# Kernel tuning notes

Measured on AMD Instinct MI355X. Metric: run time of the kernel, lower is better.

The kernel has to match this reference:

```python
import jax, jax.numpy as jnp
import numpy as np

B, N, C = 2, 384, 128
D = C // 4          # bottleneck_dim
H = 128             # time_mlp_hidden_dim


def setup_inputs() -> dict:
    key = jax.random.key(0)
    ks = jax.random.split(key, 12)
    s = 0.02
    return {
        "edge_embed": jax.random.normal(ks[0], (B, N, N, C), jnp.float32),
        "edge_mask": jax.random.randint(ks[1], (B, N, N), 0, 2, jnp.int32),
        "r3_t": jax.random.uniform(ks[2], (B,), jnp.float32),
        # linear params stored as [in, out]
        "Wg": jax.random.normal(ks[3], (C, D), jnp.float32) * s,
        "bg": jnp.zeros((D,), jnp.float32),
        "Wv": jax.random.normal(ks[4], (C, D), jnp.float32) * s,
        "bv": jnp.zeros((D,), jnp.float32),
        "Wd": jax.random.normal(ks[5], (C, D), jnp.float32) * s,
        "bd": jnp.zeros((D,), jnp.float32),
        "Wo": jax.random.normal(ks[6], (D, C), jnp.float32) * s,
        "bo": jnp.zeros((C,), jnp.float32),
        "W1": jax.random.normal(ks[7], (1, H), jnp.float32) * s,
        "b1": jnp.zeros((H,), jnp.float32),
        "W2": jax.random.normal(ks[8], (H, 2 * C), jnp.float32) * s,
        "b2": jnp.zeros((2 * C,), jnp.float32),
    }


def reference(edge_embed, edge_mask, r3_t, Wg, bg, Wv, bv, Wd, bd, Wo, bo, W1, b1, W2, b2):
    Bb, Nn, _, Cc = edge_embed.shape
    P = edge_embed.reshape(Bb, Nn * Nn, Cc)          # [B, N^2, C]
    m = (edge_mask.reshape(Bb, Nn * Nn, 1) != 0)
    mf = m.astype(P.dtype)

    fP = P @ Wg + bg                                 # [B, N^2, D]
    gP = P @ Wv + bv                                 # [B, N^2, D]
    fP = jnp.where(m, fP, jnp.asarray(-1e8, P.dtype))
    w = jax.nn.softmax(fP, axis=1)                   # softmax over all edges
    w = w * mf
    w = w / (w.sum(axis=1, keepdims=True) + 1e-8)

    V = jnp.einsum('bnd,bne->bde', w, gP)            # [B, D, D] global context

    hP = jax.nn.softmax(P @ Wd + bd, axis=2)         # softmax over channels
    O = jnp.einsum('bnd,bde->bne', hP, V)            # redistribute
    O = (O @ Wo + bo).reshape(Bb, Nn, Nn, Cc)

    # FiLM conditioned on timestep (torch GELU is exact erf form)
    t = r3_t.reshape(Bb, 1)
    t_emb = jax.nn.gelu(t @ W1 + b1, approximate=False) @ W2 + b2
    scale, shift = jnp.split(t_emb, 2, axis=-1)
    O = O * (1 + scale[:, None, None, :]) + shift[:, None, None, :]

    return edge_embed + O
```

## Files before the change

### kernel.cpp

```cpp
#include <hip/hip_runtime.h>
#include <hip/hip_bf16.h>
#include <math.h>

#define N2 147456
#define CC 128
#define TILES 2304

#define WS_VACC  0
#define WS_S     2048
#define WS_FS    2112
#define WS_SH    2368
#define WS_UPACK 2624
#define WS_B2P   6720

typedef __attribute__((ext_vector_type(8))) __bf16 bf16x8;
typedef __attribute__((ext_vector_type(4))) __bf16 bf16x4;
typedef __attribute__((ext_vector_type(4))) float f32x4;

#define MFMA16(a_, b_, c_) __builtin_amdgcn_mfma_f32_16x16x32_bf16((a_), (b_), (c_), 0, 0, 0)

__global__ __launch_bounds__(256) void k0_init(
    const float* __restrict__ r3t,
    const float* __restrict__ W1, const float* __restrict__ b1,
    const float* __restrict__ W2, const float* __restrict__ b2,
    float* __restrict__ ws)
{
    const int t = threadIdx.x, bx = blockIdx.x;
    if (bx > 0) {
        const int i = (bx - 1) * 256 + t;
        if (i < 2112) ws[i] = 0.0f;
        return;
    }
    __shared__ float h[2][128];
    {
        const int b = t >> 7, j = t & 127;
        const float x = r3t[b] * W1[j] + b1[j];
        h[b][j] = 0.5f * x * (1.0f + erff(x * 0.7071067811865475f));
    }
    __syncthreads();
    const int j2 = t;
    float acc0 = b2[j2], acc1 = b2[j2];
    for (int k = 0; k < 128; ++k) {
        const float w2 = W2[k * 256 + j2];
        acc0 += h[0][k] * w2;
        acc1 += h[1][k] * w2;
    }
    if (j2 < 128) {
        ws[WS_FS + j2]       = 1.0f + acc0;
        ws[WS_FS + 128 + j2] = 1.0f + acc1;
    } else {
        ws[WS_SH + (j2 - 128)]       = acc0;
        ws[WS_SH + 128 + (j2 - 128)] = acc1;
    }
}

__global__ __launch_bounds__(256, 3) void k1_accum(
    const float* __restrict__ P, const int* __restrict__ mask,
    const float* __restrict__ Wg, const float* __restrict__ bg,
    const float* __restrict__ Wv, const float* __restrict__ bv,
    float* __restrict__ ws)
{
    __shared__ __bf16 ef_t[32][72];
    __shared__ __bf16 gv_t[32][72];

    const int t  = threadIdx.x;
    const int b  = blockIdx.y;
    const int w  = t >> 6;
    const int l  = t & 63;
    const int lr = l & 15;
    const int lg = l >> 4;

    bf16x8 wfrag[2][2][4];
    #pragma unroll
    for (int nt = 0; nt < 2; ++nt)
      #pragma unroll
      for (int ks = 0; ks < 4; ++ks) {
        const int base = (ks * 32 + 8 * lg) * 32 + nt * 16 + lr;
        bf16x8 f0, f1;
        #pragma unroll
        for (int i = 0; i < 8; ++i) {
            f0[i] = (__bf16)Wg[base + i * 32];
            f1[i] = (__bf16)Wv[base + i * 32];
        }
        wfrag[0][nt][ks] = f0;
        wfrag[1][nt][ks] = f1;
      }
    const float bgv[2] = { bg[lr], bg[lr + 16] };
    const float bvv[2] = { bv[lr], bv[lr + 16] };

    const int mt = w >> 1, ntq = w & 1;
    f32x4 vacc = {0.f, 0.f, 0.f, 0.f};
    float accS = 0.f;
    const int sd = t >> 3, ss = t & 7;

    const float* Pb = P + (size_t)b * N2 * CC;
    const int*   mb = mask + (size_t)b * N2;

    for (int tile = blockIdx.x; tile < TILES; tile += gridDim.x) {
        const int row0 = tile * 64 + w * 16;
        const float* prow = Pb + (size_t)(row0 + lr) * CC + 8 * lg;

        bf16x8 afrag[4];
        #pragma unroll
        for (int ks = 0; ks < 4; ++ks) {
            const float4 a0 = *(const float4*)(prow + ks * 32);
            const float4 a1 = *(const float4*)(prow + ks * 32 + 4);
            bf16x8 f;
            f[0] = (__bf16)a0.x; f[1] = (__bf16)a0.y; f[2] = (__bf16)a0.z; f[3] = (__bf16)a0.w;
            f[4] = (__bf16)a1.x; f[5] = (__bf16)a1.y; f[6] = (__bf16)a1.z; f[7] = (__bf16)a1.w;
            afrag[ks] = f;
        }

        f32x4 facc0 = {0,0,0,0}, facc1 = {0,0,0,0}, gacc0 = {0,0,0,0}, gacc1 = {0,0,0,0};
        #pragma unroll
        for (int ks = 0; ks < 4; ++ks) {
            facc0 = MFMA16(afrag[ks], wfrag[0][0][ks], facc0);
            facc1 = MFMA16(afrag[ks], wfrag[0][1][ks], facc1);
            gacc0 = MFMA16(afrag[ks], wfrag[1][0][ks], gacc0);
            gacc1 = MFMA16(afrag[ks], wfrag[1][1][ks], gacc1);
        }

        const int4 mk4 = *(const int4*)&mb[row0 + lg * 4];
        const int mk[4] = { mk4.x, mk4.y, mk4.z, mk4.w };

        bf16x4 pe0, pe1, pg0, pg1;
        #pragma unroll
        for (int r = 0; r < 4; ++r) {
            pe0[r] = (__bf16)(mk[r] ? __expf(facc0[r] + bgv[0]) : 0.0f);
            pe1[r] = (__bf16)(mk[r] ? __expf(facc1[r] + bgv[1]) : 0.0f);
            pg0[r] = (__bf16)(gacc0[r] + bvv[0]);
            pg1[r] = (__bf16)(gacc1[r] + bvv[1]);
        }
        const int cbase = w * 16 + lg * 4;
        *(bf16x4*)&ef_t[lr     ][cbase] = pe0;
        *(bf16x4*)&ef_t[lr + 16][cbase] = pe1;
        *(bf16x4*)&gv_t[lr     ][cbase] = pg0;
        *(bf16x4*)&gv_t[lr + 16][cbase] = pg1;
        __syncthreads();

        #pragma unroll
        for (int ks = 0; ks < 2; ++ks) {
            const bf16x8 ea = *(const bf16x8*)&ef_t[mt  * 16 + lr][ks * 32 + 8 * lg];
            const bf16x8 gb = *(const bf16x8*)&gv_t[ntq * 16 + lr][ks * 32 + 8 * lg];
            vacc = MFMA16(ea, gb, vacc);
        }
        {
            const bf16x8 ev = *(const bf16x8*)&ef_t[sd][ss * 8];
            float s = 0.f;
            #pragma unroll
            for (int i = 0; i < 8; ++i) s += (float)ev[i];
            accS += s;
        }
        __syncthreads();
    }

    #pragma unroll
    for (int r = 0; r < 4; ++r) {
        const int d = mt * 16 + lg * 4 + r;
        const int e = ntq * 16 + lr;
        atomicAdd(ws + WS_VACC + b * 1024 + d * 32 + e, vacc[r]);
    }
    accS += __shfl_xor(accS, 1);
    accS += __shfl_xor(accS, 2);
    accS += __shfl_xor(accS, 4);
    if (ss == 0) atomicAdd(ws + WS_S + b * 32 + sd, accS);
}

__global__ __launch_bounds__(256) void k2_mid(
    const float* __restrict__ Wo, const float* __restrict__ bo,
    float* __restrict__ ws)
{
    __shared__ float V[1024];
    __shared__ float wo[32][128];
    __shared__ float fs[128];
    const int t = threadIdx.x, b = blockIdx.x;

    if (t < 128) fs[t] = ws[WS_FS + b * 128 + t];
    #pragma unroll
    for (int i = 0; i < 4; ++i) {
        const int idx = t + i * 256;
        const int d = idx >> 5;
        const float s = ws[WS_S + b * 32 + d];
        V[idx] = ws[WS_VACC + b * 1024 + idx] / (s * (1.0f + 1e-8f));
    }
    #pragma unroll
    for (int i = 0; i < 4; ++i) {
        const int j = t + i * 256;
        ((float4*)&wo[0][0])[j] = ((const float4*)Wo)[j];
    }
    __syncthreads();

    const int c = t & 127, dh = t >> 7;
    float wcol[32];
    #pragma unroll
    for (int e = 0; e < 32; ++e) wcol[e] = wo[e][c];
    const float fsc = fs[c];
    if (dh == 0) ws[WS_B2P + b * 128 + c] = bo[c] * fsc + ws[WS_SH + b * 128 + c];

    __bf16* dst = (__bf16*)(ws + WS_UPACK);
    #pragma unroll
    for (int dd = 0; dd < 16; ++dd) {
        const int d = dh * 16 + dd;
        float acc = 0.0f;
        #pragma unroll
        for (int e = 0; e < 32; ++e) acc += V[d * 32 + e] * wcol[e];
        acc *= fsc;
        const int lg = d >> 3, ii = d & 7, nt = c >> 4, lr = c & 15;
        dst[(((size_t)b * 8 + nt) * 64 + (lg * 16 + lr)) * 8 + ii] = (__bf16)acc;
    }
}

__global__ __launch_bounds__(256, 3) void k3_out(
    const float* __restrict__ P,
    const float* __restrict__ Wd, const float* __restrict__ bd,
    const float* __restrict__ ws, float* __restrict__ out)
{
    __shared__ __bf16 h_t[64][40];

    const int t  = threadIdx.x;
    const int b  = blockIdx.y;
    const int w  = t >> 6, l = t & 63, lr = l & 15, lg = l >> 4;

    bf16x8 ufrag[8];
    {
        const bf16x8* up = (const bf16x8*)(ws + WS_UPACK) + (size_t)b * 512 + l;
        #pragma unroll
        for (int nt = 0; nt < 8; ++nt) ufrag[nt] = up[nt * 64];
    }
    float b2v[8][4];
    #pragma unroll
    for (int nt = 0; nt < 8; ++nt) {
        const float4 v = *(const float4*)(ws + WS_B2P + b * 128 + nt * 16 + lg * 4);
        b2v[nt][0] = v.x; b2v[nt][1] = v.y; b2v[nt][2] = v.z; b2v[nt][3] = v.w;
    }
    bf16x8 wdfrag[2][4];
    #pragma unroll
    for (int nt = 0; nt < 2; ++nt)
      #pragma unroll
      for (int ks = 0; ks < 4; ++ks) {
        const int base = (ks * 32 + 8 * lg) * 32 + nt * 16 + lr;
        bf16x8 f;
        #pragma unroll
        for (int i = 0; i < 8; ++i) f[i] = (__bf16)Wd[base + i * 32];
        wdfrag[nt][ks] = f;
      }
    float bdv[8];
    #pragma unroll
    for (int r = 0; r < 4; ++r) {
        bdv[r]     = bd[lg * 4 + r];
        bdv[4 + r] = bd[16 + lg * 4 + r];
    }

    const float* Pb = P + (size_t)b * N2 * CC;
    float*       Ob = out + (size_t)b * N2 * CC;

    for (int tile = TILES - 1 - blockIdx.x; tile >= 0; tile -= gridDim.x) {
        const int row0 = tile * 64 + w * 16;
        const size_t rbase = (size_t)(row0 + lr) * CC;
        const float* prow = Pb + rbase + 8 * lg;

        bf16x8 afrag[4];
        #pragma unroll
        for (int ks = 0; ks < 4; ++ks) {
            const float4 a0 = *(const float4*)(prow + ks * 32);
            const float4 a1 = *(const float4*)(prow + ks * 32 + 4);
            bf16x8 f;
            f[0] = (__bf16)a0.x; f[1] = (__bf16)a0.y; f[2] = (__bf16)a0.z; f[3] = (__bf16)a0.w;
            f[4] = (__bf16)a1.x; f[5] = (__bf16)a1.y; f[6] = (__bf16)a1.z; f[7] = (__bf16)a1.w;
            afrag[ks] = f;
        }

        f32x4 dacc0 = {0,0,0,0}, dacc1 = {0,0,0,0};
        #pragma unroll
        for (int ks = 0; ks < 4; ++ks) {
            dacc0 = MFMA16(wdfrag[0][ks], afrag[ks], dacc0);
            dacc1 = MFMA16(wdfrag[1][ks], afrag[ks], dacc1);
        }

        float v[8];
        #pragma unroll
        for (int r = 0; r < 4; ++r) {
            v[r]     = dacc0[r] + bdv[r];
            v[4 + r] = dacc1[r] + bdv[4 + r];
        }
        float m = v[0];
        #pragma unroll
        for (int j = 1; j < 8; ++j) m = fmaxf(m, v[j]);
        m = fmaxf(m, __shfl_xor(m, 16));
        m = fmaxf(m, __shfl_xor(m, 32));
        float e[8], s = 0.f;
        #pragma unroll
        for (int j = 0; j < 8; ++j) { e[j] = __expf(v[j] - m); s += e[j]; }
        s += __shfl_xor(s, 16);
        s += __shfl_xor(s, 32);
        const float inv = 1.0f / s;

        bf16x4 h0, h1;
        #pragma unroll
        for (int r = 0; r < 4; ++r) {
            h0[r] = (__bf16)(e[r] * inv);
            h1[r] = (__bf16)(e[4 + r] * inv);
        }
        const int hrow = w * 16 + lr;
        *(bf16x4*)&h_t[hrow][lg * 4]      = h0;
        *(bf16x4*)&h_t[hrow][16 + lg * 4] = h1;
        const bf16x8 hf = *(const bf16x8*)&h_t[hrow][8 * lg];

        #pragma unroll
        for (int nt = 0; nt < 8; ++nt) {
            f32x4 ci;
            ci[0] = b2v[nt][0]; ci[1] = b2v[nt][1]; ci[2] = b2v[nt][2]; ci[3] = b2v[nt][3];
            const f32x4 oacc = MFMA16(ufrag[nt], hf, ci);
            const size_t off = rbase + nt * 16 + lg * 4;
            const float4 p4 = *(const float4*)(Pb + off);
            float4 o4;
            o4.x = p4.x + oacc[0]; o4.y = p4.y + oacc[1];
            o4.z = p4.z + oacc[2]; o4.w = p4.w + oacc[3];
            *(float4*)(Ob + off) = o4;
        }
    }
}

extern "C" void kernel_launch(void* const* d_in, const int* in_sizes, int n_in,
                              void* d_out, int out_size, void* d_ws, size_t ws_size,
                              hipStream_t stream) {
    const float* P   = (const float*)d_in[0];
    const int*   msk = (const int*)d_in[1];
    const float* r3t = (const float*)d_in[2];
    const float* Wg  = (const float*)d_in[3];
    const float* bg  = (const float*)d_in[4];
    const float* Wv  = (const float*)d_in[5];
    const float* bv  = (const float*)d_in[6];
    const float* Wd  = (const float*)d_in[7];
    const float* bd  = (const float*)d_in[8];
    const float* Wo  = (const float*)d_in[9];
    const float* bo  = (const float*)d_in[10];
    const float* W1  = (const float*)d_in[11];
    const float* b1  = (const float*)d_in[12];
    const float* W2  = (const float*)d_in[13];
    const float* b2  = (const float*)d_in[14];
    float* ws  = (float*)d_ws;
    float* out = (float*)d_out;

    hipLaunchKernelGGL(k0_init,  dim3(10),      dim3(256), 0, stream, r3t, W1, b1, W2, b2, ws);
    hipLaunchKernelGGL(k1_accum, dim3(384, 2),  dim3(256), 0, stream, P, msk, Wg, bg, Wv, bv, ws);
    hipLaunchKernelGGL(k2_mid,   dim3(2),       dim3(256), 0, stream, Wo, bo, ws);
    hipLaunchKernelGGL(k3_out,   dim3(768, 2),  dim3(256), 0, stream, P, Wd, bd, ws, out);
}
```

Before: 117.6 us.

## Fold time-MLP into mid kernel, memset workspace, prefetch next P tile in output kernel

Removes the separate init kernel: the workspace is zeroed with hipMemsetAsync and the FiLM time-MLP (GELU plus W2 projection) is now computed inside k2_mid into shared memory. In k3_out, the P rows for the next tile are loaded into registers while the current tile is converted and processed, so global load latency overlaps with MFMA and softmax work. The prefetch raises register pressure under the 3-blocks-per-CU launch bound. The memset may still count as a launch of its own.

```diff
diff --git a/kernel.cpp b/kernel.cpp
--- a/kernel.cpp
+++ b/kernel.cpp
@@ -8,8 +8,6 @@
 
 #define WS_VACC  0
 #define WS_S     2048
-#define WS_FS    2112
-#define WS_SH    2368
 #define WS_UPACK 2624
 #define WS_B2P   6720
 
@@ -18,41 +16,6 @@
 typedef __attribute__((ext_vector_type(4))) float f32x4;
 
 #define MFMA16(a_, b_, c_) __builtin_amdgcn_mfma_f32_16x16x32_bf16((a_), (b_), (c_), 0, 0, 0)
-
-__global__ __launch_bounds__(256) void k0_init(
-    const float* __restrict__ r3t,
-    const float* __restrict__ W1, const float* __restrict__ b1,
-    const float* __restrict__ W2, const float* __restrict__ b2,
-    float* __restrict__ ws)
-{
-    const int t = threadIdx.x, bx = blockIdx.x;
-    if (bx > 0) {
-        const int i = (bx - 1) * 256 + t;
-        if (i < 2112) ws[i] = 0.0f;
-        return;
-    }
-    __shared__ float h[2][128];
-    {
-        const int b = t >> 7, j = t & 127;
-        const float x = r3t[b] * W1[j] + b1[j];
-        h[b][j] = 0.5f * x * (1.0f + erff(x * 0.7071067811865475f));
-    }
-    __syncthreads();
-    const int j2 = t;
-    float acc0 = b2[j2], acc1 = b2[j2];
-    for (int k = 0; k < 128; ++k) {
-        const float w2 = W2[k * 256 + j2];
-        acc0 += h[0][k] * w2;
-        acc1 += h[1][k] * w2;
-    }
-    if (j2 < 128) {
-        ws[WS_FS + j2]       = 1.0f + acc0;
-        ws[WS_FS + 128 + j2] = 1.0f + acc1;
-    } else {
-        ws[WS_SH + (j2 - 128)]       = acc0;
-        ws[WS_SH + 128 + (j2 - 128)] = acc1;
-    }
-}
 
 __global__ __launch_bounds__(256, 3) void k1_accum(
     const float* __restrict__ P, const int* __restrict__ mask,
@@ -167,15 +130,23 @@
 }
 
 __global__ __launch_bounds__(256) void k2_mid(
+    const float* __restrict__ r3t,
+    const float* __restrict__ W1, const float* __restrict__ b1,
+    const float* __restrict__ W2, const float* __restrict__ b2,
     const float* __restrict__ Wo, const float* __restrict__ bo,
     float* __restrict__ ws)
 {
     __shared__ float V[1024];
     __shared__ float wo[32][128];
+    __shared__ float h[128];
     __shared__ float fs[128];
+    __shared__ float sh[128];
     const int t = threadIdx.x, b = blockIdx.x;
 
-    if (t < 128) fs[t] = ws[WS_FS + b * 128 + t];
+    if (t < 128) {
+        const float x = r3t[b] * W1[t] + b1[t];
+        h[t] = 0.5f * x * (1.0f + erff(x * 0.7071067811865475f));
+    }
     #pragma unroll
     for (int i = 0; i < 4; ++i) {
         const int idx = t + i * 256;
@@ -190,12 +161,20 @@
     }
     __syncthreads();
 
+    {
+        float acc = b2[t];
+        for (int k = 0; k < 128; ++k) acc += h[k] * W2[k * 256 + t];
+        if (t < 128) fs[t] = 1.0f + acc;
+        else         sh[t - 128] = acc;
+    }
+    __syncthreads();
+
     const int c = t & 127, dh = t >> 7;
     float wcol[32];
     #pragma unroll
     for (int e = 0; e < 32; ++e) wcol[e] = wo[e][c];
     const float fsc = fs[c];
-    if (dh == 0) ws[WS_B2P + b * 128 + c] = bo[c] * fsc + ws[WS_SH + b * 128 + c];
+    if (dh == 0) ws[WS_B2P + b * 128 + c] = bo[c] * fsc + sh[c];
 
     __bf16* dst = (__bf16*)(ws + WS_UPACK);
     #pragma unroll
@@ -253,21 +232,40 @@
 
     const float* Pb = P + (size_t)b * N2 * CC;
     float*       Ob = out + (size_t)b * N2 * CC;
-
-    for (int tile = TILES - 1 - blockIdx.x; tile >= 0; tile -= gridDim.x) {
+    const int step = gridDim.x;
+
+    int tile = TILES - 1 - blockIdx.x;
+    float4 a4[8];
+    {
+        const float* prow = Pb + (size_t)(tile * 64 + w * 16 + lr) * CC + 8 * lg;
+        #pragma unroll
+        for (int ks = 0; ks < 4; ++ks) {
+            a4[2 * ks]     = *(const float4*)(prow + ks * 32);
+            a4[2 * ks + 1] = *(const float4*)(prow + ks * 32 + 4);
+        }
+    }
+
+    for (; tile >= 0; tile -= step) {
         const int row0 = tile * 64 + w * 16;
         const size_t rbase = (size_t)(row0 + lr) * CC;
-        const float* prow = Pb + rbase + 8 * lg;
 
         bf16x8 afrag[4];
         #pragma unroll
         for (int ks = 0; ks < 4; ++ks) {
-            const float4 a0 = *(const float4*)(prow + ks * 32);
-            const float4 a1 = *(const float4*)(prow + ks * 32 + 4);
+            const float4 a0 = a4[2 * ks], a1 = a4[2 * ks + 1];
             bf16x8 f;
             f[0] = (__bf16)a0.x; f[1] = (__bf16)a0.y; f[2] = (__bf16)a0.z; f[3] = (__bf16)a0.w;
             f[4] = (__bf16)a1.x; f[5] = (__bf16)a1.y; f[6] = (__bf16)a1.z; f[7] = (__bf16)a1.w;
             afrag[ks] = f;
+        }
+        const int ntile = tile - step;
+        if (ntile >= 0) {
+            const float* prow = Pb + (size_t)(ntile * 64 + w * 16 + lr) * CC + 8 * lg;
+            #pragma unroll
+            for (int ks = 0; ks < 4; ++ks) {
+                a4[2 * ks]     = *(const float4*)(prow + ks * 32);
+                a4[2 * ks + 1] = *(const float4*)(prow + ks * 32 + 4);
+            }
         }
 
         f32x4 dacc0 = {0,0,0,0}, dacc1 = {0,0,0,0};
@@ -342,8 +340,8 @@
     float* ws  = (float*)d_ws;
     float* out = (float*)d_out;
 
-    hipLaunchKernelGGL(k0_init,  dim3(10),      dim3(256), 0, stream, r3t, W1, b1, W2, b2, ws);
+    hipMemsetAsync(ws, 0, 2112 * sizeof(float), stream);
     hipLaunchKernelGGL(k1_accum, dim3(384, 2),  dim3(256), 0, stream, P, msk, Wg, bg, Wv, bv, ws);
-    hipLaunchKernelGGL(k2_mid,   dim3(2),       dim3(256), 0, stream, Wo, bo, ws);
+    hipLaunchKernelGGL(k2_mid,   dim3(2),       dim3(256), 0, stream, r3t, W1, b1, W2, b2, Wo, bo, ws);
     hipLaunchKernelGGL(k3_out,   dim3(768, 2),  dim3(256), 0, stream, P, Wd, bd, ws, out);
 }
```

After: 143.3 us. +21.8%, slower.

## Accumulate V directly from MFMA output registers, removing per-tile LDS transpose

Applied to the files above, without the earlier changes.

The accumulation kernel no longer stages the exp-weights and value projections through shared memory with two barriers per tile. It feeds the projection accumulators straight into a 16x16x16 bf16 MFMA, using each wave's output layout as the K dimension, so every wave keeps its own 32x32 partial of V. Row sums are kept in registers as well. The per-wave partials are reduced through shared memory once at the end, at the cost of more accumulator registers and a larger shared-memory buffer for that final reduction.

```diff
diff --git a/kernel.cpp b/kernel.cpp
--- a/kernel.cpp
+++ b/kernel.cpp
@@ -16,8 +16,21 @@
 typedef __attribute__((ext_vector_type(8))) __bf16 bf16x8;
 typedef __attribute__((ext_vector_type(4))) __bf16 bf16x4;
 typedef __attribute__((ext_vector_type(4))) float f32x4;
+typedef __attribute__((ext_vector_type(4))) short short4v;
 
 #define MFMA16(a_, b_, c_) __builtin_amdgcn_mfma_f32_16x16x32_bf16((a_), (b_), (c_), 0, 0, 0)
+
+static __device__ inline f32x4 mfma_k16(bf16x4 a, bf16x4 b, f32x4 c) {
+#if __has_builtin(__builtin_amdgcn_mfma_f32_16x16x16_bf16)
+    return __builtin_amdgcn_mfma_f32_16x16x16_bf16(a, b, c, 0, 0, 0);
+#elif __has_builtin(__builtin_amdgcn_mfma_f32_16x16x16bf16_1k)
+    return __builtin_amdgcn_mfma_f32_16x16x16bf16_1k(
+        __builtin_bit_cast(short4v, a), __builtin_bit_cast(short4v, b), c, 0, 0, 0);
+#else
+    asm("v_mfma_f32_16x16x16_bf16 %0, %1, %2, %0" : "+v"(c) : "v"(a), "v"(b));
+    return c;
+#endif
+}
 
 __global__ __launch_bounds__(256) void k0_init(
     const float* __restrict__ r3t,
@@ -60,8 +73,8 @@
     const float* __restrict__ Wv, const float* __restrict__ bv,
     float* __restrict__ ws)
 {
-    __shared__ __bf16 ef_t[32][72];
-    __shared__ __bf16 gv_t[32][72];
+    __shared__ float red[4][1024];
+    __shared__ float red_s[4][32];
 
     const int t  = threadIdx.x;
     const int b  = blockIdx.y;
@@ -88,10 +101,8 @@
     const float bgv[2] = { bg[lr], bg[lr + 16] };
     const float bvv[2] = { bv[lr], bv[lr + 16] };
 
-    const int mt = w >> 1, ntq = w & 1;
-    f32x4 vacc = {0.f, 0.f, 0.f, 0.f};
-    float accS = 0.f;
-    const int sd = t >> 3, ss = t & 7;
+    f32x4 vq00 = {0,0,0,0}, vq01 = {0,0,0,0}, vq10 = {0,0,0,0}, vq11 = {0,0,0,0};
+    float s0 = 0.f, s1 = 0.f;
 
     const float* Pb = P + (size_t)b * N2 * CC;
     const int*   mb = mask + (size_t)b * N2;
@@ -131,39 +142,42 @@
             pg0[r] = (__bf16)(gacc0[r] + bvv[0]);
             pg1[r] = (__bf16)(gacc1[r] + bvv[1]);
         }
-        const int cbase = w * 16 + lg * 4;
-        *(bf16x4*)&ef_t[lr     ][cbase] = pe0;
-        *(bf16x4*)&ef_t[lr + 16][cbase] = pe1;
-        *(bf16x4*)&gv_t[lr     ][cbase] = pg0;
-        *(bf16x4*)&gv_t[lr + 16][cbase] = pg1;
-        __syncthreads();
-
-        #pragma unroll
-        for (int ks = 0; ks < 2; ++ks) {
-            const bf16x8 ea = *(const bf16x8*)&ef_t[mt  * 16 + lr][ks * 32 + 8 * lg];
-            const bf16x8 gb = *(const bf16x8*)&gv_t[ntq * 16 + lr][ks * 32 + 8 * lg];
-            vacc = MFMA16(ea, gb, vacc);
-        }
-        {
-            const bf16x8 ev = *(const bf16x8*)&ef_t[sd][ss * 8];
-            float s = 0.f;
-            #pragma unroll
-            for (int i = 0; i < 8; ++i) s += (float)ev[i];
-            accS += s;
-        }
-        __syncthreads();
-    }
+
+        #pragma unroll
+        for (int r = 0; r < 4; ++r) {
+            s0 += (float)pe0[r];
+            s1 += (float)pe1[r];
+        }
+
+        vq00 = mfma_k16(pe0, pg0, vq00);
+        vq01 = mfma_k16(pe0, pg1, vq01);
+        vq10 = mfma_k16(pe1, pg0, vq10);
+        vq11 = mfma_k16(pe1, pg1, vq11);
+    }
+
+    s0 += __shfl_xor(s0, 16); s0 += __shfl_xor(s0, 32);
+    s1 += __shfl_xor(s1, 16); s1 += __shfl_xor(s1, 32);
 
     #pragma unroll
     for (int r = 0; r < 4; ++r) {
-        const int d = mt * 16 + lg * 4 + r;
-        const int e = ntq * 16 + lr;
-        atomicAdd(ws + WS_VACC + b * 1024 + d * 32 + e, vacc[r]);
-    }
-    accS += __shfl_xor(accS, 1);
-    accS += __shfl_xor(accS, 2);
-    accS += __shfl_xor(accS, 4);
-    if (ss == 0) atomicAdd(ws + WS_S + b * 32 + sd, accS);
+        red[w][(     4 * lg + r) * 32 +      lr] = vq00[r];
+        red[w][(     4 * lg + r) * 32 + 16 + lr] = vq01[r];
+        red[w][(16 + 4 * lg + r) * 32 +      lr] = vq10[r];
+        red[w][(16 + 4 * lg + r) * 32 + 16 + lr] = vq11[r];
+    }
+    if (lg == 0) { red_s[w][lr] = s0; red_s[w][16 + lr] = s1; }
+    __syncthreads();
+
+    #pragma unroll
+    for (int i = 0; i < 4; ++i) {
+        const int idx = t + i * 256;
+        const float v = red[0][idx] + red[1][idx] + red[2][idx] + red[3][idx];
+        atomicAdd(ws + WS_VACC + b * 1024 + idx, v);
+    }
+    if (t < 32) {
+        const float sv = red_s[0][t] + red_s[1][t] + red_s[2][t] + red_s[3][t];
+        atomicAdd(ws + WS_S + b * 32 + t, sv);
+    }
 }
 
 __global__ __launch_bounds__(256) void k2_mid(
```

Measured after the change: 111.0 us (median of 2 runs). -5.6%, faster.
